# Optimization experiments

Hardware: AMD Instinct MI355X
Metric: run time of the kernel (lower is better)

Reference implementation:

```python
import jax, jax.numpy as jnp
import numpy as np

N = 50000
E = 800000
H = 8          # attention heads
C = 16         # per-head channels (128 // 8)
D = 128        # in_channels == num_hidden_channels
L = 2          # num_layers
NEG_SLOPE = 0.2
LN_EPS = 1e-12


def setup_inputs() -> dict:
    key = jax.random.key(0)
    ks = jax.random.split(key, 8)
    x = jax.random.normal(ks[0], (N, D), dtype=jnp.float32)
    edge_index = jax.random.randint(ks[1], (2, E), 0, N).astype(jnp.int64)
    W = jax.random.normal(ks[2], (L, D, D), dtype=jnp.float32) * 0.1
    att = jax.random.normal(ks[3], (L, H, C), dtype=jnp.float32) * 0.1
    bias = jnp.zeros((L, D), dtype=jnp.float32)
    out_W = jax.random.normal(ks[4], (D, D), dtype=jnp.float32) * 0.1
    out_b = jnp.zeros((D,), dtype=jnp.float32)
    ln_g = jnp.ones((D,), dtype=jnp.float32)
    ln_b = jnp.zeros((D,), dtype=jnp.float32)
    return {"x": x, "edge_index": edge_index, "W": W, "att": att, "bias": bias,
            "out_W": out_W, "out_b": out_b, "ln_g": ln_g, "ln_b": ln_b,
            "num_trg_nodes": 25000}


def gatv2_conv(x, src, dst, W_l, a_l, b_l):
    # share_weights=True: same linear map for source and target nodes
    h = (x @ W_l).reshape(N, H, C)               # [N,H,C]
    hs = h[src]                                  # [E,H,C] gather source
    hd = h[dst]                                  # [E,H,C] gather target
    e = jax.nn.leaky_relu(hs + hd, NEG_SLOPE)    # GATv2: LeakyReLU before attention vector
    logits = jnp.einsum('ehc,hc->eh', e, a_l)    # [E,H]
    # segment softmax over edges grouped by destination node
    seg_max = jax.ops.segment_max(logits, dst, num_segments=N)   # [N,H]
    ex = jnp.exp(logits - seg_max[dst])
    seg_sum = jax.ops.segment_sum(ex, dst, num_segments=N)       # [N,H]
    alpha = ex / (seg_sum[dst] + 1e-16)                          # [E,H]
    msg = (hs * alpha[..., None]).reshape(E, H * C)              # weighted messages
    out = jax.ops.segment_sum(msg, dst, num_segments=N)          # [N,H*C]
    return out + b_l


def reference(x, edge_index, W, att, bias, out_W, out_b, ln_g, ln_b, num_trg_nodes):
    src = edge_index[0]
    dst = edge_index[1]
    for i in range(L):
        x = gatv2_conv(x, src, dst, W[i], att[i], bias[i])
        if i != L - 1:
            # eval mode: dropout is identity; torch nn.GELU is exact erf gelu
            x = jax.nn.gelu(x, approximate=False)
    # output head: Linear -> LayerNorm(eps=1e-12) -> Dropout(identity in eval)
    y = x[:num_trg_nodes] @ out_W + out_b
    mu = jnp.mean(y, axis=-1, keepdims=True)
    var = jnp.mean(jnp.square(y - mu), axis=-1, keepdims=True)
    y = (y - mu) / jnp.sqrt(var + LN_EPS) * ln_g + ln_b
    return y
```

## Files before the change

### kernel.cpp

```cpp
#include <hip/hip_runtime.h>
#include <math.h>


#define D 128
#define H 8
#define C 16
#define NBIN 256

typedef __attribute__((ext_vector_type(8))) short bf16x8v;
typedef __attribute__((ext_vector_type(4))) float f32x4v;

static __device__ __forceinline__ float bf2f(unsigned int u16) {
    union { unsigned int i; float f; } x; x.i = u16 << 16; return x.f;
}
static __device__ __forceinline__ unsigned short f2bf(float f) {
    union { float f; unsigned int i; } x; x.f = f;
    unsigned int r = x.i + 0x7fffu + ((x.i >> 16) & 1u);
    return (unsigned short)(r >> 16);
}
static __device__ __forceinline__ float gelu_f(float v) {
    return 0.5f * v * (1.0f + erff(v * 0.70710678118654752f));
}
static __device__ __forceinline__ float exp2_hw(float x) {
    float r;
    asm("v_exp_f32 %0, %1" : "=v"(r) : "v"(x));
    return r;
}
#define DPP_ADD(v, ctrl) \
    (v) += __builtin_bit_cast(float, __builtin_amdgcn_update_dpp( \
        0, __builtin_bit_cast(int, (v)), (ctrl), 0xf, 0xf, true))

template<int IN_BF, int OUT_BF, int GELU>
static __device__ __forceinline__ void gemm_body(
    int bid, const void* __restrict__ Xv, const unsigned short* __restrict__ Wt,
    const float* __restrict__ bias, void* __restrict__ Outv, int nrows)
{
    const int t  = threadIdx.x;
    const int l  = t & 63;
    const int wv = t >> 6;
    const int rh = wv >> 1;
    const int chh = wv & 1;
    const int g  = l >> 4;
    const int r  = l & 15;
    const int m0 = bid * 32 + rh * 16;
    const int row = m0 + r;
    const bool rv = row < nrows;
    const uint4* Wt4 = reinterpret_cast<const uint4*>(Wt);

    bf16x8v afrag[4];
#pragma unroll
    for (int kk = 0; kk < 4; ++kk) {
        int kg = kk * 4 + g;
        float v[8];
        if (IN_BF) {
            uint4 q = make_uint4(0, 0, 0, 0);
            if (rv) q = reinterpret_cast<const uint4*>(Xv)[(size_t)row * 16 + kg];
            if (GELU) {
                unsigned int qq[4] = {q.x, q.y, q.z, q.w};
#pragma unroll
                for (int j = 0; j < 4; ++j) {
                    v[2 * j]     = gelu_f(bf2f(qq[j] & 0xffffu));
                    v[2 * j + 1] = gelu_f(bf2f(qq[j] >> 16));
                }
                short pk[8];
#pragma unroll
                for (int j = 0; j < 8; ++j) pk[j] = (short)f2bf(v[j]);
                afrag[kk] = *reinterpret_cast<bf16x8v*>(pk);
            } else {
                afrag[kk] = __builtin_bit_cast(bf16x8v, q);
            }
        } else {
            float4 a = make_float4(0.f, 0.f, 0.f, 0.f), b = a;
            if (rv) {
                a = reinterpret_cast<const float4*>(Xv)[(size_t)row * 32 + kg * 2];
                b = reinterpret_cast<const float4*>(Xv)[(size_t)row * 32 + kg * 2 + 1];
            }
            v[0] = a.x; v[1] = a.y; v[2] = a.z; v[3] = a.w;
            v[4] = b.x; v[5] = b.y; v[6] = b.z; v[7] = b.w;
            if (GELU) {
#pragma unroll
                for (int j = 0; j < 8; ++j) v[j] = gelu_f(v[j]);
            }
            short pk[8];
#pragma unroll
            for (int j = 0; j < 8; ++j) pk[j] = (short)f2bf(v[j]);
            afrag[kk] = *reinterpret_cast<bf16x8v*>(pk);
        }
    }

    f32x4v acc[4];
#pragma unroll
    for (int ct = 0; ct < 4; ++ct) acc[ct] = (f32x4v){0.f, 0.f, 0.f, 0.f};

    bf16x8v bA[4], bB[4];
#pragma unroll
    for (int ct = 0; ct < 4; ++ct)
        bA[ct] = __builtin_bit_cast(bf16x8v, Wt4[((chh * 4 + ct) * 16 + r) * 16 + g]);

#pragma unroll
    for (int kk = 0; kk < 4; ++kk) {
        if (kk < 3) {
            int kgn = (kk + 1) * 4 + g;
#pragma unroll
            for (int ct = 0; ct < 4; ++ct) {
                bf16x8v v = __builtin_bit_cast(bf16x8v,
                    Wt4[((chh * 4 + ct) * 16 + r) * 16 + kgn]);
                if (kk & 1) bA[ct] = v; else bB[ct] = v;
            }
        }
#pragma unroll
        for (int ct = 0; ct < 4; ++ct) {
            bf16x8v b = (kk & 1) ? bB[ct] : bA[ct];
            acc[ct] = __builtin_amdgcn_mfma_f32_16x16x32_bf16(afrag[kk], b, acc[ct], 0, 0, 0);
        }
    }

#pragma unroll
    for (int ct = 0; ct < 4; ++ct) {
        int col = (chh * 4 + ct) * 16 + r;
        float bj = bias ? bias[col] : 0.f;
#pragma unroll
        for (int i = 0; i < 4; ++i) {
            int rr = m0 + g * 4 + i;
            if (rr < nrows) {
                float val = acc[ct][i] + bj;
                if (OUT_BF)
                    reinterpret_cast<unsigned short*>(Outv)[(size_t)rr * 128 + col] = f2bf(val);
                else
                    reinterpret_cast<float*>(Outv)[(size_t)rr * 128 + col] = val;
            }
        }
    }
}

__global__ __launch_bounds__(256) void gemm_head_ln(
    const void* __restrict__ Xv, const unsigned short* __restrict__ Wt,
    const float* __restrict__ outb, const float* __restrict__ lng,
    const float* __restrict__ lnb, float* __restrict__ Out, int nrows)
{
    const int t  = threadIdx.x;
    const int l  = t & 63;
    const int wv = t >> 6;
    const int g  = l >> 4;
    const int r  = l & 15;
    const int m0 = blockIdx.x * 64;
    const int row = m0 + wv * 16 + r;
    const bool rv = row < nrows;
    const uint4* Wt4 = reinterpret_cast<const uint4*>(Wt);

    bf16x8v afrag[4];
#pragma unroll
    for (int kk = 0; kk < 4; ++kk) {
        int kg = kk * 4 + g;
        uint4 q = make_uint4(0, 0, 0, 0);
        if (rv) q = reinterpret_cast<const uint4*>(Xv)[(size_t)row * 16 + kg];
        afrag[kk] = __builtin_bit_cast(bf16x8v, q);
    }

    f32x4v acc[8];
#pragma unroll
    for (int ct = 0; ct < 8; ++ct) acc[ct] = (f32x4v){0.f, 0.f, 0.f, 0.f};

#pragma unroll
    for (int kk = 0; kk < 4; ++kk) {
        int kg = kk * 4 + g;
#pragma unroll
        for (int ct = 0; ct < 8; ++ct) {
            bf16x8v b = __builtin_bit_cast(bf16x8v, Wt4[(ct * 16 + r) * 16 + kg]);
            acc[ct] = __builtin_amdgcn_mfma_f32_16x16x32_bf16(afrag[kk], b, acc[ct], 0, 0, 0);
        }
    }

    float gmm[8], bbb[8];
#pragma unroll
    for (int ct = 0; ct < 8; ++ct) {
        gmm[ct] = lng[ct * 16 + r];
        bbb[ct] = lnb[ct * 16 + r];
    }

#pragma unroll
    for (int i = 0; i < 4; ++i) {
        int rr = m0 + wv * 16 + g * 4 + i;
        if (rr >= nrows) continue;
        float v[8];
        float s = 0.f;
#pragma unroll
        for (int ct = 0; ct < 8; ++ct) {
            v[ct] = acc[ct][i] + outb[ct * 16 + r];
            s += v[ct];
        }
        DPP_ADD(s, 0xB1); DPP_ADD(s, 0x4E); DPP_ADD(s, 0x141); DPP_ADD(s, 0x140);
        float mu = s * (1.f / 128.f);
        float q = 0.f;
#pragma unroll
        for (int ct = 0; ct < 8; ++ct) {
            float dd = v[ct] - mu;
            q += dd * dd;
        }
        DPP_ADD(q, 0xB1); DPP_ADD(q, 0x4E); DPP_ADD(q, 0x141); DPP_ADD(q, 0x140);
        float inv = rsqrtf(q * (1.f / 128.f) + 1e-12f);
#pragma unroll
        for (int ct = 0; ct < 8; ++ct)
            Out[(size_t)rr * 128 + ct * 16 + r] = (v[ct] - mu) * inv * gmm[ct] + bbb[ct];
    }
}

__global__ __launch_bounds__(256) void prep_kernel(
    const float* __restrict__ W, const float* __restrict__ outW,
    unsigned short* __restrict__ wbf,
    const int* __restrict__ dst, int* __restrict__ bh,
    int E, int chunk, int nblk)
{
    __shared__ char smem[128 * 17 * 2];
    int t = threadIdx.x;
    if (blockIdx.x < 24) {
        unsigned short (*tile)[17] = reinterpret_cast<unsigned short (*)[17]>(smem);
        int blk = blockIdx.x;
        int mat = blk >> 3, s = blk & 7;
        const float* src = (mat < 2) ? (W + (size_t)mat * D * D) : outW;
        unsigned short* dstp = wbf + (size_t)mat * D * D;
        int n0 = s * 16;
#pragma unroll
        for (int it = 0; it < 8; ++it) {
            int idx = it * 256 + t;
            int k = idx >> 4, n = idx & 15;
            tile[k][n] = f2bf(src[k * D + n0 + n]);
        }
        __syncthreads();
#pragma unroll
        for (int it = 0; it < 8; ++it) {
            int idx = it * 256 + t;
            int n = idx >> 7, k = idx & 127;
            dstp[(size_t)(n0 + n) * D + k] = tile[k][n];
        }
    } else {
        int* h = reinterpret_cast<int*>(smem);
        int b = blockIdx.x - 24;
        h[t] = 0;
        __syncthreads();
        int lo = b * chunk, hi = min(E, lo + chunk);
        int i = lo + t * 4;
        for (; i + 3 < hi; i += 1024) {
            int4 q = *reinterpret_cast<const int4*>(dst + i);
            atomicAdd(&h[q.x >> 8], 1);
            atomicAdd(&h[q.y >> 8], 1);
            atomicAdd(&h[q.z >> 8], 1);
            atomicAdd(&h[q.w >> 8], 1);
        }
        for (; i < hi; ++i) atomicAdd(&h[dst[i] >> 8], 1);
        __syncthreads();
        bh[t * nblk + b] = h[t];
    }
}

__global__ __launch_bounds__(256) void bin_scan(
    int* __restrict__ bh, int* __restrict__ tot, int nblk)
{
    __shared__ int sh[256];
    int bin = blockIdx.x, t = threadIdx.x;
    int v = (t < nblk) ? bh[bin * nblk + t] : 0;
    sh[t] = v;
    __syncthreads();
#pragma unroll
    for (int off = 1; off < 256; off <<= 1) {
        int x = (t >= off) ? sh[t - off] : 0;
        __syncthreads();
        sh[t] += x;
        __syncthreads();
    }
    if (t < nblk) bh[bin * nblk + t] = sh[t] - v;
    if (t == 255) tot[bin] = sh[255];
}

__global__ __launch_bounds__(256) void scatter_gemm0(
    const int* __restrict__ dst, const int* __restrict__ src,
    const int* __restrict__ bh, const int* __restrict__ tot,
    unsigned int* __restrict__ bout, int E, int chunk, int nblk,
    const float* __restrict__ x, const unsigned short* __restrict__ wbf,
    void* __restrict__ hbuf, int nrows)
{
    __shared__ int sh[NBIN];
    __shared__ int cur[NBIN];
    int t = threadIdx.x;
    if (blockIdx.x < nblk) {
        int b = blockIdx.x;
        int tv = tot[t];
        sh[t] = tv;
        __syncthreads();
#pragma unroll
        for (int off = 1; off < 256; off <<= 1) {
            int xq = (t >= off) ? sh[t - off] : 0;
            __syncthreads();
            sh[t] += xq;
            __syncthreads();
        }
        cur[t] = (sh[t] - tv) + bh[t * nblk + b];
        __syncthreads();
        int lo = b * chunk, hi = min(E, lo + chunk);
        int i = lo + t * 4;
        for (; i + 3 < hi; i += 1024) {
            int4 dq = *reinterpret_cast<const int4*>(dst + i);
            int4 sq = *reinterpret_cast<const int4*>(src + i);
            int p0 = atomicAdd(&cur[dq.x >> 8], 1);
            bout[p0] = ((unsigned)sq.x << 8) | (dq.x & 255);
            int p1 = atomicAdd(&cur[dq.y >> 8], 1);
            bout[p1] = ((unsigned)sq.y << 8) | (dq.y & 255);
            int p2 = atomicAdd(&cur[dq.z >> 8], 1);
            bout[p2] = ((unsigned)sq.z << 8) | (dq.z & 255);
            int p3 = atomicAdd(&cur[dq.w >> 8], 1);
            bout[p3] = ((unsigned)sq.w << 8) | (dq.w & 255);
        }
        for (; i < hi; ++i) {
            int d = dst[i];
            int p = atomicAdd(&cur[d >> 8], 1);
            bout[p] = ((unsigned)src[i] << 8) | (d & 255);
        }
    } else {
        gemm_body<0, 1, 0>(blockIdx.x - nblk, x, wbf, nullptr, hbuf, nrows);
    }
}

__global__ __launch_bounds__(256) void gemm_l1(
    const void* __restrict__ Xv, const unsigned short* __restrict__ Wt,
    void* __restrict__ Outv, int nrows)
{
    gemm_body<1, 1, 1>(blockIdx.x, Xv, Wt, nullptr, Outv, nrows);
}

__global__ __launch_bounds__(256) void fill_fused(
    const unsigned int* __restrict__ bout, const int* __restrict__ tot,
    int* __restrict__ rowptr, int* __restrict__ slist, int N, int E)
{
    __shared__ int sh[NBIN];
    __shared__ int cnt[NBIN];
    __shared__ int cur[NBIN];
    int b = blockIdx.x, t = threadIdx.x;

    int tv = tot[t];
    sh[t] = tv;
    __syncthreads();
#pragma unroll
    for (int off = 1; off < 256; off <<= 1) {
        int x = (t >= off) ? sh[t - off] : 0;
        __syncthreads();
        sh[t] += x;
        __syncthreads();
    }
    int hi = sh[b];
    int lo = hi - tot[b];

    cnt[t] = 0;
    __syncthreads();
    for (int i = lo + t; i < hi; i += 256) atomicAdd(&cnt[bout[i] & 255], 1);
    __syncthreads();

    int cv = cnt[t];
    sh[t] = cv;
    __syncthreads();
#pragma unroll
    for (int off = 1; off < 256; off <<= 1) {
        int x = (t >= off) ? sh[t - off] : 0;
        __syncthreads();
        sh[t] += x;
        __syncthreads();
    }
    int start = lo + sh[t] - cv;
    int d0 = b * 256 + t;
    if (d0 < N) rowptr[d0] = start;
    if (b == (int)gridDim.x - 1 && t == 255) rowptr[N] = E;
    cur[t] = start;
    __syncthreads();

    for (int i = lo + t; i < hi; i += 256) {
        unsigned e = bout[i];
        int p = atomicAdd(&cur[e & 255], 1);
        slist[p] = (int)(e >> 8);
    }
}

#define PROC(u, k) \
    float h##k##x = bf2f((u) & 0xffffu), h##k##y = bf2f((u) >> 16); \
    float v##k##0 = h##k##x + hdx, v##k##1 = h##k##y + hdy; \
    float p##k = fmaf(aw1.x, v##k##0, fmaf(aw2.x, fabsf(v##k##0), \
                 fmaf(aw1.y, v##k##1, aw2.y * fabsf(v##k##1)))); \
    DPP_ADD(p##k, 0xB1); DPP_ADD(p##k, 0x4E); DPP_ADD(p##k, 0x141); \
    float e##k = exp2_hw(p##k);

#define QUAD_BODY(U0, U1, U2, U3) \
    { PROC(U0, 0) PROC(U1, 1) PROC(U2, 2) PROC(U3, 3) \
      ssum += (e0 + e1) + (e2 + e3); \
      accx = fmaf(e0, h0x, fmaf(e1, h1x, fmaf(e2, h2x, fmaf(e3, h3x, accx)))); \
      accy = fmaf(e0, h0y, fmaf(e1, h1y, fmaf(e2, h2y, fmaf(e3, h3y, accy)))); }

__global__ __launch_bounds__(256) void aggregate(
    const unsigned int* __restrict__ Hm,
    const int* __restrict__ rowptr, const int* __restrict__ slist,
    const float* __restrict__ att, const float* __restrict__ bias,
    unsigned int* __restrict__ Outv, int n)
{
    int wid  = threadIdx.x >> 6;
    int lane = threadIdx.x & 63;
    int d = blockIdx.x * 4 + wid;
    if (d >= n) return;

    int beg = __builtin_amdgcn_readfirstlane(rowptr[d]);
    int end = __builtin_amdgcn_readfirstlane(rowptr[d + 1]);

    unsigned int ud = Hm[((unsigned)d << 6) | lane];
    float hdx = bf2f(ud & 0xffffu), hdy = bf2f(ud >> 16);
    float2 aw = reinterpret_cast<const float2*>(att)[lane];
    float2 aw1, aw2;
    aw1.x = aw.x * 0.86561702453f;
    aw1.y = aw.y * 0.86561702453f;
    aw2.x = aw.x * 0.57707801636f;
    aw2.y = aw.y * 0.57707801636f;

    float ssum = 0.f, accx = 0.f, accy = 0.f;

    int nfull = (end - beg) >> 2;
    int ii = beg;
    unsigned cu0, cu1, cu2, cu3;
    if (nfull) {
        cu0 = Hm[((unsigned)slist[ii]     << 6) | lane];
        cu1 = Hm[((unsigned)slist[ii + 1] << 6) | lane];
        cu2 = Hm[((unsigned)slist[ii + 2] << 6) | lane];
        cu3 = Hm[((unsigned)slist[ii + 3] << 6) | lane];
    }
    for (int q = 1; q < nfull; ++q) {
        int j = ii + 4;
        unsigned nu0 = Hm[((unsigned)slist[j]     << 6) | lane];
        unsigned nu1 = Hm[((unsigned)slist[j + 1] << 6) | lane];
        unsigned nu2 = Hm[((unsigned)slist[j + 2] << 6) | lane];
        unsigned nu3 = Hm[((unsigned)slist[j + 3] << 6) | lane];
        QUAD_BODY(cu0, cu1, cu2, cu3)
        cu0 = nu0; cu1 = nu1; cu2 = nu2; cu3 = nu3;
        ii = j;
    }
    if (nfull) {
        QUAD_BODY(cu0, cu1, cu2, cu3)
        ii += 4;
    }
    for (; ii < end; ++ii) {
        unsigned u0 = Hm[((unsigned)slist[ii] << 6) | lane];
        PROC(u0, 9)
        ssum += e9;
        accx = fmaf(e9, h9x, accx);
        accy = fmaf(e9, h9y, accy);
    }

    float inv = 1.f / (ssum + 1e-16f);
    float2 bv = reinterpret_cast<const float2*>(bias)[lane];
    float ox = accx * inv + bv.x;
    float oy = accy * inv + bv.y;
    Outv[((unsigned)d << 6) | lane] =
        (unsigned int)f2bf(ox) | ((unsigned int)f2bf(oy) << 16);
}

extern "C" void kernel_launch(void* const* d_in, const int* in_sizes, int n_in,
                              void* d_out, int out_size, void* d_ws, size_t ws_size,
                              hipStream_t stream)
{
    const float* x    = (const float*)d_in[0];
    const int*   edge = (const int*)d_in[1];
    const float* W    = (const float*)d_in[2];
    const float* att  = (const float*)d_in[3];
    const float* bias = (const float*)d_in[4];
    const float* outW = (const float*)d_in[5];
    const float* outb = (const float*)d_in[6];
    const float* lng  = (const float*)d_in[7];
    const float* lnb  = (const float*)d_in[8];

    const int N  = in_sizes[0] / D;
    const int E  = in_sizes[1] / 2;
    const int NT = out_size / D;

    const int* srcp = edge;
    const int* dstp = edge + E;

    auto align256 = [](size_t v) { return (v + 255) & ~(size_t)255; };
    auto cdiv = [](int a, int b) { return (a + b - 1) / b; };

    const int CHUNK = (cdiv(E, 256) + 3) & ~3;
    const int NBLK  = cdiv(E, CHUNK);
    const int NBKT  = cdiv(N, 256);
    const int NG    = cdiv(N, 32);

    char* wp = (char*)d_ws;
    size_t off = 0;
    void* hbuf   = (void*)(wp + off); off += align256((size_t)N * D * 2);
    void* xbuf   = (void*)(wp + off); off += align256((size_t)N * D * 2);
    unsigned short* wbf = (unsigned short*)(wp + off); off += align256((size_t)3 * D * D * 2);
    int*  rowptr = (int*)(wp + off);  off += align256((size_t)(N + 1) * 4);
    int*  slist  = (int*)(wp + off);  off += align256((size_t)E * 4);
    unsigned int* bout = (unsigned int*)(wp + off); off += align256((size_t)E * 4);
    int*  bh     = (int*)(wp + off);  off += align256((size_t)NBIN * NBLK * 4);
    int*  tot    = (int*)(wp + off);  off += align256((size_t)NBIN * 4);
    (void)n_in; (void)ws_size;

    prep_kernel<<<24 + NBLK, 256, 0, stream>>>(W, outW, wbf, dstp, bh, E, CHUNK, NBLK);
    bin_scan<<<NBIN, 256, 0, stream>>>(bh, tot, NBLK);
    scatter_gemm0<<<NBLK + NG, 256, 0, stream>>>(dstp, srcp, bh, tot, bout,
                                                 E, CHUNK, NBLK, x, wbf, hbuf, N);
    fill_fused<<<NBKT, 256, 0, stream>>>(bout, tot, rowptr, slist, N, E);
    aggregate<<<cdiv(N, 4), 256, 0, stream>>>((unsigned int*)hbuf, rowptr, slist,
                                              att, bias, (unsigned int*)xbuf, N);
    gemm_l1<<<NG, 256, 0, stream>>>(xbuf, wbf + D * D, hbuf, N);
    aggregate<<<cdiv(N, 4), 256, 0, stream>>>((unsigned int*)hbuf, rowptr, slist,
                                              att + H * C, bias + D, (unsigned int*)xbuf, N);
    gemm_head_ln<<<cdiv(NT, 64), 256, 0, stream>>>(xbuf, wbf + 2 * D * D, outb,
                                                   lng, lnb, (float*)d_out, NT);
}
```

Before: 151.0 us.

## Merge graph-build and first GEMM kernels into one cooperative persistent kernel

The four preprocessing launches (weight conversion and histogram, bin scan, scatter plus layer-0 GEMM, CSR fill) are combined into a single cooperative kernel that separates the phases with grid-wide syncs and loops over virtual blocks. The separate kernels are kept as a fallback when the cooperative launch fails. The aim is to remove three launch gaps and kernel-boundary drains. In exchange, grid.sync adds cost, and a grid capped at occupancy×256 and at most 2048 blocks may serialize work that used to spread across more blocks.

```diff
diff --git a/kernel.cpp b/kernel.cpp
--- a/kernel.cpp
+++ b/kernel.cpp
@@ -1,5 +1,8 @@
 #include <hip/hip_runtime.h>
+#include <hip/hip_cooperative_groups.h>
 #include <math.h>
+
+namespace cg = cooperative_groups;
 
 
 #define D 128
@@ -133,6 +136,237 @@
     }
 }
 
+static __device__ void prep_body(
+    int vb, const float* __restrict__ W, const float* __restrict__ outW,
+    unsigned short* __restrict__ wbf,
+    const int* __restrict__ dst, int* __restrict__ bh,
+    int E, int chunk, int nblk, char* smem)
+{
+    int t = threadIdx.x;
+    if (vb < 24) {
+        unsigned short (*tile)[17] = reinterpret_cast<unsigned short (*)[17]>(smem);
+        int mat = vb >> 3, s = vb & 7;
+        const float* src = (mat < 2) ? (W + (size_t)mat * D * D) : outW;
+        unsigned short* dstp = wbf + (size_t)mat * D * D;
+        int n0 = s * 16;
+#pragma unroll
+        for (int it = 0; it < 8; ++it) {
+            int idx = it * 256 + t;
+            int k = idx >> 4, n = idx & 15;
+            tile[k][n] = f2bf(src[k * D + n0 + n]);
+        }
+        __syncthreads();
+#pragma unroll
+        for (int it = 0; it < 8; ++it) {
+            int idx = it * 256 + t;
+            int n = idx >> 7, k = idx & 127;
+            dstp[(size_t)(n0 + n) * D + k] = tile[k][n];
+        }
+    } else {
+        int* h = reinterpret_cast<int*>(smem);
+        int b = vb - 24;
+        h[t] = 0;
+        __syncthreads();
+        int lo = b * chunk, hi = min(E, lo + chunk);
+        int i = lo + t * 4;
+        for (; i + 3 < hi; i += 1024) {
+            int4 q = *reinterpret_cast<const int4*>(dst + i);
+            atomicAdd(&h[q.x >> 8], 1);
+            atomicAdd(&h[q.y >> 8], 1);
+            atomicAdd(&h[q.z >> 8], 1);
+            atomicAdd(&h[q.w >> 8], 1);
+        }
+        for (; i < hi; ++i) atomicAdd(&h[dst[i] >> 8], 1);
+        __syncthreads();
+        bh[t * nblk + b] = h[t];
+    }
+    __syncthreads();
+}
+
+static __device__ void binscan_body(
+    int bin, int* __restrict__ bh, int* __restrict__ tot, int nblk, char* smem)
+{
+    int* sh = reinterpret_cast<int*>(smem);
+    int t = threadIdx.x;
+    int v = (t < nblk) ? bh[bin * nblk + t] : 0;
+    sh[t] = v;
+    __syncthreads();
+#pragma unroll
+    for (int off = 1; off < 256; off <<= 1) {
+        int x = (t >= off) ? sh[t - off] : 0;
+        __syncthreads();
+        sh[t] += x;
+        __syncthreads();
+    }
+    if (t < nblk) bh[bin * nblk + t] = sh[t] - v;
+    if (t == 255) tot[bin] = sh[255];
+    __syncthreads();
+}
+
+static __device__ void scatter_body(
+    int b, const int* __restrict__ dst, const int* __restrict__ src,
+    const int* __restrict__ bh, const int* __restrict__ tot,
+    unsigned int* __restrict__ bout, int E, int chunk, int nblk, char* smem)
+{
+    int* sh  = reinterpret_cast<int*>(smem);
+    int* cur = sh + NBIN;
+    int t = threadIdx.x;
+    int tv = tot[t];
+    sh[t] = tv;
+    __syncthreads();
+#pragma unroll
+    for (int off = 1; off < 256; off <<= 1) {
+        int xq = (t >= off) ? sh[t - off] : 0;
+        __syncthreads();
+        sh[t] += xq;
+        __syncthreads();
+    }
+    cur[t] = (sh[t] - tv) + bh[t * nblk + b];
+    __syncthreads();
+    int lo = b * chunk, hi = min(E, lo + chunk);
+    int i = lo + t * 4;
+    for (; i + 3 < hi; i += 1024) {
+        int4 dq = *reinterpret_cast<const int4*>(dst + i);
+        int4 sq = *reinterpret_cast<const int4*>(src + i);
+        int p0 = atomicAdd(&cur[dq.x >> 8], 1);
+        bout[p0] = ((unsigned)sq.x << 8) | (dq.x & 255);
+        int p1 = atomicAdd(&cur[dq.y >> 8], 1);
+        bout[p1] = ((unsigned)sq.y << 8) | (dq.y & 255);
+        int p2 = atomicAdd(&cur[dq.z >> 8], 1);
+        bout[p2] = ((unsigned)sq.z << 8) | (dq.z & 255);
+        int p3 = atomicAdd(&cur[dq.w >> 8], 1);
+        bout[p3] = ((unsigned)sq.w << 8) | (dq.w & 255);
+    }
+    for (; i < hi; ++i) {
+        int d = dst[i];
+        int p = atomicAdd(&cur[d >> 8], 1);
+        bout[p] = ((unsigned)src[i] << 8) | (d & 255);
+    }
+    __syncthreads();
+}
+
+static __device__ void fill_body(
+    int b, const unsigned int* __restrict__ bout, const int* __restrict__ tot,
+    int* __restrict__ rowptr, int* __restrict__ slist, int N, int E, int nbkt,
+    char* smem)
+{
+    int* sh  = reinterpret_cast<int*>(smem);
+    int* cnt = sh + NBIN;
+    int* cur = cnt + NBIN;
+    int t = threadIdx.x;
+
+    int tv = tot[t];
+    sh[t] = tv;
+    __syncthreads();
+#pragma unroll
+    for (int off = 1; off < 256; off <<= 1) {
+        int x = (t >= off) ? sh[t - off] : 0;
+        __syncthreads();
+        sh[t] += x;
+        __syncthreads();
+    }
+    int hi = sh[b];
+    int lo = hi - tot[b];
+
+    cnt[t] = 0;
+    __syncthreads();
+    for (int i = lo + t; i < hi; i += 256) atomicAdd(&cnt[bout[i] & 255], 1);
+    __syncthreads();
+
+    int cv = cnt[t];
+    sh[t] = cv;
+    __syncthreads();
+#pragma unroll
+    for (int off = 1; off < 256; off <<= 1) {
+        int x = (t >= off) ? sh[t - off] : 0;
+        __syncthreads();
+        sh[t] += x;
+        __syncthreads();
+    }
+    int start = lo + sh[t] - cv;
+    int d0 = b * 256 + t;
+    if (d0 < N) rowptr[d0] = start;
+    if (b == nbkt - 1 && t == 255) rowptr[N] = E;
+    cur[t] = start;
+    __syncthreads();
+
+    for (int i = lo + t; i < hi; i += 256) {
+        unsigned e = bout[i];
+        int p = atomicAdd(&cur[e & 255], 1);
+        slist[p] = (int)(e >> 8);
+    }
+    __syncthreads();
+}
+
+struct MegaArgs {
+    const float* W; const float* outW; unsigned short* wbf;
+    const int* dst; const int* src; int* bh; int* tot;
+    unsigned int* bout; int* rowptr; int* slist;
+    const float* x; void* hbuf;
+    int E, N, chunk, nblk, nbkt, ng;
+};
+
+__global__ __launch_bounds__(256) void mega_build(MegaArgs a)
+{
+    cg::grid_group grid = cg::this_grid();
+    __shared__ char smem[4608];
+
+    for (int vb = blockIdx.x; vb < 24 + a.nblk; vb += gridDim.x)
+        prep_body(vb, a.W, a.outW, a.wbf, a.dst, a.bh, a.E, a.chunk, a.nblk, smem);
+    grid.sync();
+    for (int vb = blockIdx.x; vb < NBIN; vb += gridDim.x)
+        binscan_body(vb, a.bh, a.tot, a.nblk, smem);
+    grid.sync();
+    for (int vb = blockIdx.x; vb < a.nblk + a.ng; vb += gridDim.x) {
+        if (vb < a.nblk)
+            scatter_body(vb, a.dst, a.src, a.bh, a.tot, a.bout, a.E, a.chunk, a.nblk, smem);
+        else
+            gemm_body<0, 1, 0>(vb - a.nblk, a.x, a.wbf, nullptr, a.hbuf, a.N);
+        __syncthreads();
+    }
+    grid.sync();
+    for (int vb = blockIdx.x; vb < a.nbkt; vb += gridDim.x)
+        fill_body(vb, a.bout, a.tot, a.rowptr, a.slist, a.N, a.E, a.nbkt, smem);
+}
+
+__global__ __launch_bounds__(256) void prep_kernel(
+    const float* W, const float* outW, unsigned short* wbf,
+    const int* dst, int* bh, int E, int chunk, int nblk)
+{
+    __shared__ char smem[4608];
+    prep_body(blockIdx.x, W, outW, wbf, dst, bh, E, chunk, nblk, smem);
+}
+__global__ __launch_bounds__(256) void bin_scan_k(int* bh, int* tot, int nblk)
+{
+    __shared__ char smem[4608];
+    binscan_body(blockIdx.x, bh, tot, nblk, smem);
+}
+__global__ __launch_bounds__(256) void scatter_gemm0_k(
+    const int* dst, const int* src, const int* bh, const int* tot,
+    unsigned int* bout, int E, int chunk, int nblk,
+    const float* x, const unsigned short* wbf, void* hbuf, int nrows)
+{
+    __shared__ char smem[4608];
+    if ((int)blockIdx.x < nblk)
+        scatter_body(blockIdx.x, dst, src, bh, tot, bout, E, chunk, nblk, smem);
+    else
+        gemm_body<0, 1, 0>(blockIdx.x - nblk, x, wbf, nullptr, hbuf, nrows);
+}
+__global__ __launch_bounds__(256) void fill_k(
+    const unsigned int* bout, const int* tot, int* rowptr, int* slist,
+    int N, int E, int nbkt)
+{
+    __shared__ char smem[4608];
+    fill_body(blockIdx.x, bout, tot, rowptr, slist, N, E, nbkt, smem);
+}
+
+__global__ __launch_bounds__(256) void gemm_l1(
+    const void* __restrict__ Xv, const unsigned short* __restrict__ Wt,
+    void* __restrict__ Outv, int nrows)
+{
+    gemm_body<1, 1, 1>(blockIdx.x, Xv, Wt, nullptr, Outv, nrows);
+}
+
 __global__ __launch_bounds__(256) void gemm_head_ln(
     const void* __restrict__ Xv, const unsigned short* __restrict__ Wt,
     const float* __restrict__ outb, const float* __restrict__ lng,
@@ -202,179 +436,6 @@
 #pragma unroll
         for (int ct = 0; ct < 8; ++ct)
             Out[(size_t)rr * 128 + ct * 16 + r] = (v[ct] - mu) * inv * gmm[ct] + bbb[ct];
-    }
-}
-
-__global__ __launch_bounds__(256) void prep_kernel(
-    const float* __restrict__ W, const float* __restrict__ outW,
-    unsigned short* __restrict__ wbf,
-    const int* __restrict__ dst, int* __restrict__ bh,
-    int E, int chunk, int nblk)
-{
-    __shared__ char smem[128 * 17 * 2];
-    int t = threadIdx.x;
-    if (blockIdx.x < 24) {
-        unsigned short (*tile)[17] = reinterpret_cast<unsigned short (*)[17]>(smem);
-        int blk = blockIdx.x;
-        int mat = blk >> 3, s = blk & 7;
-        const float* src = (mat < 2) ? (W + (size_t)mat * D * D) : outW;
-        unsigned short* dstp = wbf + (size_t)mat * D * D;
-        int n0 = s * 16;
-#pragma unroll
-        for (int it = 0; it < 8; ++it) {
-            int idx = it * 256 + t;
-            int k = idx >> 4, n = idx & 15;
-            tile[k][n] = f2bf(src[k * D + n0 + n]);
-        }
-        __syncthreads();
-#pragma unroll
-        for (int it = 0; it < 8; ++it) {
-            int idx = it * 256 + t;
-            int n = idx >> 7, k = idx & 127;
-            dstp[(size_t)(n0 + n) * D + k] = tile[k][n];
-        }
-    } else {
-        int* h = reinterpret_cast<int*>(smem);
-        int b = blockIdx.x - 24;
-        h[t] = 0;
-        __syncthreads();
-        int lo = b * chunk, hi = min(E, lo + chunk);
-        int i = lo + t * 4;
-        for (; i + 3 < hi; i += 1024) {
-            int4 q = *reinterpret_cast<const int4*>(dst + i);
-            atomicAdd(&h[q.x >> 8], 1);
-            atomicAdd(&h[q.y >> 8], 1);
-            atomicAdd(&h[q.z >> 8], 1);
-            atomicAdd(&h[q.w >> 8], 1);
-        }
-        for (; i < hi; ++i) atomicAdd(&h[dst[i] >> 8], 1);
-        __syncthreads();
-        bh[t * nblk + b] = h[t];
-    }
-}
-
-__global__ __launch_bounds__(256) void bin_scan(
-    int* __restrict__ bh, int* __restrict__ tot, int nblk)
-{
-    __shared__ int sh[256];
-    int bin = blockIdx.x, t = threadIdx.x;
-    int v = (t < nblk) ? bh[bin * nblk + t] : 0;
-    sh[t] = v;
-    __syncthreads();
-#pragma unroll
-    for (int off = 1; off < 256; off <<= 1) {
-        int x = (t >= off) ? sh[t - off] : 0;
-        __syncthreads();
-        sh[t] += x;
-        __syncthreads();
-    }
-    if (t < nblk) bh[bin * nblk + t] = sh[t] - v;
-    if (t == 255) tot[bin] = sh[255];
-}
-
-__global__ __launch_bounds__(256) void scatter_gemm0(
-    const int* __restrict__ dst, const int* __restrict__ src,
-    const int* __restrict__ bh, const int* __restrict__ tot,
-    unsigned int* __restrict__ bout, int E, int chunk, int nblk,
-    const float* __restrict__ x, const unsigned short* __restrict__ wbf,
-    void* __restrict__ hbuf, int nrows)
-{
-    __shared__ int sh[NBIN];
-    __shared__ int cur[NBIN];
-    int t = threadIdx.x;
-    if (blockIdx.x < nblk) {
-        int b = blockIdx.x;
-        int tv = tot[t];
-        sh[t] = tv;
-        __syncthreads();
-#pragma unroll
-        for (int off = 1; off < 256; off <<= 1) {
-            int xq = (t >= off) ? sh[t - off] : 0;
-            __syncthreads();
-            sh[t] += xq;
-            __syncthreads();
-        }
-        cur[t] = (sh[t] - tv) + bh[t * nblk + b];
-        __syncthreads();
-        int lo = b * chunk, hi = min(E, lo + chunk);
-        int i = lo + t * 4;
-        for (; i + 3 < hi; i += 1024) {
-            int4 dq = *reinterpret_cast<const int4*>(dst + i);
-            int4 sq = *reinterpret_cast<const int4*>(src + i);
-            int p0 = atomicAdd(&cur[dq.x >> 8], 1);
-            bout[p0] = ((unsigned)sq.x << 8) | (dq.x & 255);
-            int p1 = atomicAdd(&cur[dq.y >> 8], 1);
-            bout[p1] = ((unsigned)sq.y << 8) | (dq.y & 255);
-            int p2 = atomicAdd(&cur[dq.z >> 8], 1);
-            bout[p2] = ((unsigned)sq.z << 8) | (dq.z & 255);
-            int p3 = atomicAdd(&cur[dq.w >> 8], 1);
-            bout[p3] = ((unsigned)sq.w << 8) | (dq.w & 255);
-        }
-        for (; i < hi; ++i) {
-            int d = dst[i];
-            int p = atomicAdd(&cur[d >> 8], 1);
-            bout[p] = ((unsigned)src[i] << 8) | (d & 255);
-        }
-    } else {
-        gemm_body<0, 1, 0>(blockIdx.x - nblk, x, wbf, nullptr, hbuf, nrows);
-    }
-}
-
-__global__ __launch_bounds__(256) void gemm_l1(
-    const void* __restrict__ Xv, const unsigned short* __restrict__ Wt,
-    void* __restrict__ Outv, int nrows)
-{
-    gemm_body<1, 1, 1>(blockIdx.x, Xv, Wt, nullptr, Outv, nrows);
-}
-
-__global__ __launch_bounds__(256) void fill_fused(
-    const unsigned int* __restrict__ bout, const int* __restrict__ tot,
-    int* __restrict__ rowptr, int* __restrict__ slist, int N, int E)
-{
-    __shared__ int sh[NBIN];
-    __shared__ int cnt[NBIN];
-    __shared__ int cur[NBIN];
-    int b = blockIdx.x, t = threadIdx.x;
-
-    int tv = tot[t];
-    sh[t] = tv;
-    __syncthreads();
-#pragma unroll
-    for (int off = 1; off < 256; off <<= 1) {
-        int x = (t >= off) ? sh[t - off] : 0;
-        __syncthreads();
-        sh[t] += x;
-        __syncthreads();
-    }
-    int hi = sh[b];
-    int lo = hi - tot[b];
-
-    cnt[t] = 0;
-    __syncthreads();
-    for (int i = lo + t; i < hi; i += 256) atomicAdd(&cnt[bout[i] & 255], 1);
-    __syncthreads();
-
-    int cv = cnt[t];
-    sh[t] = cv;
-    __syncthreads();
-#pragma unroll
-    for (int off = 1; off < 256; off <<= 1) {
-        int x = (t >= off) ? sh[t - off] : 0;
-        __syncthreads();
-        sh[t] += x;
-        __syncthreads();
-    }
-    int start = lo + sh[t] - cv;
-    int d0 = b * 256 + t;
-    if (d0 < N) rowptr[d0] = start;
-    if (b == (int)gridDim.x - 1 && t == 255) rowptr[N] = E;
-    cur[t] = start;
-    __syncthreads();
-
-    for (int i = lo + t; i < hi; i += 256) {
-        unsigned e = bout[i];
-        int p = atomicAdd(&cur[e & 255], 1);
-        slist[p] = (int)(e >> 8);
     }
 }
 
@@ -497,11 +558,33 @@
     int*  tot    = (int*)(wp + off);  off += align256((size_t)NBIN * 4);
     (void)n_in; (void)ws_size;
 
-    prep_kernel<<<24 + NBLK, 256, 0, stream>>>(W, outW, wbf, dstp, bh, E, CHUNK, NBLK);
-    bin_scan<<<NBIN, 256, 0, stream>>>(bh, tot, NBLK);
-    scatter_gemm0<<<NBLK + NG, 256, 0, stream>>>(dstp, srcp, bh, tot, bout,
-                                                 E, CHUNK, NBLK, x, wbf, hbuf, N);
-    fill_fused<<<NBKT, 256, 0, stream>>>(bout, tot, rowptr, slist, N, E);
+    MegaArgs ma;
+    ma.W = W; ma.outW = outW; ma.wbf = wbf;
+    ma.dst = dstp; ma.src = srcp; ma.bh = bh; ma.tot = tot;
+    ma.bout = bout; ma.rowptr = rowptr; ma.slist = slist;
+    ma.x = x; ma.hbuf = hbuf;
+    ma.E = E; ma.N = N; ma.chunk = CHUNK; ma.nblk = NBLK;
+    ma.nbkt = NBKT; ma.ng = NG;
+
+    bool coop_done = false;
+    int occ = 0;
+    if (hipOccupancyMaxActiveBlocksPerMultiprocessor(&occ, mega_build, 256, 0)
+            == hipSuccess && occ > 0) {
+        int grid = occ * 256;
+        if (grid > 2048) grid = 2048;
+        void* args[] = { (void*)&ma };
+        if (hipLaunchCooperativeKernel(mega_build, dim3(grid), dim3(256),
+                                       args, 0, stream) == hipSuccess)
+            coop_done = true;
+    }
+    if (!coop_done) {
+        prep_kernel<<<24 + NBLK, 256, 0, stream>>>(W, outW, wbf, dstp, bh, E, CHUNK, NBLK);
+        bin_scan_k<<<NBIN, 256, 0, stream>>>(bh, tot, NBLK);
+        scatter_gemm0_k<<<NBLK + NG, 256, 0, stream>>>(dstp, srcp, bh, tot, bout,
+                                                       E, CHUNK, NBLK, x, wbf, hbuf, N);
+        fill_k<<<NBKT, 256, 0, stream>>>(bout, tot, rowptr, slist, N, E, NBKT);
+    }
+
     aggregate<<<cdiv(N, 4), 256, 0, stream>>>((unsigned int*)hbuf, rowptr, slist,
                                               att, bias, (unsigned int*)xbuf, N);
     gemm_l1<<<NG, 256, 0, stream>>>(xbuf, wbf + D * D, hbuf, N);
```

Result: slower. 315.0 us (+108.6%).
